# Optimization experiments

Hardware: AMD Instinct MI355X
Metric: run time of the kernel (lower is better)

Reference implementation:

```python
import jax, jax.numpy as jnp
import numpy as np

DIM = 768
NUM_HEADS = 12
HEAD_DIM = DIM // NUM_HEADS
ROPE_BASE = 10000.0


def _rope_angles(height, width, head_dim, base):
    # 2D RoPE: first half of head_dim rotates with the row (y) position,
    # second half with the column (x) position.
    half = head_dim // 2            # dims per spatial axis
    quarter = half // 2             # rotation pair count per axis
    inv_freq = 1.0 / (base ** (jnp.arange(0, half, 2, dtype=jnp.float32) / half))  # [quarter]
    ys = jnp.arange(height, dtype=jnp.float32)
    xs = jnp.arange(width, dtype=jnp.float32)
    ang_y = ys[:, None] * inv_freq  # [H, quarter]
    ang_x = xs[:, None] * inv_freq  # [W, quarter]
    ay = jnp.broadcast_to(ang_y[:, None, :], (height, width, quarter)).reshape(height * width, quarter)
    ax = jnp.broadcast_to(ang_x[None, :, :], (height, width, quarter)).reshape(height * width, quarter)
    return ay, ax


def _rotate(t, ang):
    # t: [B, nh, N, half]; ang: [N, quarter]. Interleaved pair rotation.
    c, s = jnp.cos(ang), jnp.sin(ang)
    t1, t2 = t[..., 0::2], t[..., 1::2]
    r1 = t1 * c - t2 * s
    r2 = t1 * s + t2 * c
    return jnp.stack([r1, r2], axis=-1).reshape(t.shape)


def apply_2d_rope(t, height, width, base):
    # t: [B, nh, N, head_dim]
    hd = t.shape[-1]
    half = hd // 2
    ay, ax = _rope_angles(height, width, hd, base)
    return jnp.concatenate([_rotate(t[..., :half], ay), _rotate(t[..., half:], ax)], axis=-1)


def setup_inputs() -> dict:
    key = jax.random.key(0)
    ks = jax.random.split(key, 5)
    B, N = 16, 32 * 32
    x = jax.random.normal(ks[0], (B, N, DIM), dtype=jnp.float32)
    qkv_w = jax.random.normal(ks[1], (3 * DIM, DIM), dtype=jnp.float32) * (1.0 / np.sqrt(DIM))
    qkv_b = jnp.zeros((3 * DIM,), dtype=jnp.float32)
    proj_w = jax.random.normal(ks[2], (DIM, DIM), dtype=jnp.float32) * (1.0 / np.sqrt(DIM))
    proj_b = jnp.zeros((DIM,), dtype=jnp.float32)
    return {"x": x, "qkv_w": qkv_w, "qkv_b": qkv_b, "proj_w": proj_w,
            "proj_b": proj_b, "height": 32, "width": 32}


def reference(x, qkv_w, qkv_b, proj_w, proj_b, height, width):
    B, N, C = x.shape
    scale = 1.0 / np.sqrt(HEAD_DIM)
    qkv = x @ qkv_w.T + qkv_b                      # [B, N, 3*C]
    qkv = qkv.reshape(B, N, 3, NUM_HEADS, HEAD_DIM).transpose(2, 0, 3, 1, 4)
    q, k, v = qkv[0], qkv[1], qkv[2]               # [B, nh, N, hd]
    q = apply_2d_rope(q, height, width, ROPE_BASE)
    k = apply_2d_rope(k, height, width, ROPE_BASE)
    attn = jnp.einsum('bhnd,bhmd->bhnm', q, k) * scale
    attn = jax.nn.softmax(attn, axis=-1)
    out = jnp.einsum('bhnm,bhmd->bhnd', attn, v)   # [B, nh, N, hd]
    out = out.transpose(0, 2, 1, 3).reshape(B, N, C)
    return out @ proj_w.T + proj_b
```

## Files before the change

kernel.cpp:

```cpp
#include <hip/hip_runtime.h>
#include <hip/hip_bf16.h>

typedef _Float16 f16;
typedef _Float16 half8 __attribute__((ext_vector_type(8)));
typedef _Float16 half4 __attribute__((ext_vector_type(4)));
typedef float f32x4 __attribute__((ext_vector_type(4)));
typedef unsigned short u16;
typedef unsigned int u32;

#define AS_GLOBAL __attribute__((address_space(1)))
#define AS_LDS    __attribute__((address_space(3)))

static __device__ __forceinline__ f32x4 mfma_k32(half8 a, half8 b, f32x4 c) {
  return __builtin_amdgcn_mfma_f32_16x16x32_f16(a, b, c, 0, 0, 0);
}

static __device__ __forceinline__ void glds16(const void* g, void* l) {
  __builtin_amdgcn_global_load_lds((const AS_GLOBAL u32*)(unsigned long long)g,
                                   (AS_LDS u32*)l, 16, 0, 0);
}

__global__ __launch_bounds__(256) void cvt_kernel(const float* __restrict__ src,
                                                  f16* __restrict__ dst, int n) {
  long i = ((long)blockIdx.x * 256 + threadIdx.x) * 8;
  if (i + 8 <= n) {
    const float4 a = *(const float4*)(src + i);
    const float4 b = *(const float4*)(src + i + 4);
    union { uint4 v; f16 h[8]; } o;
    o.h[0] = (f16)a.x; o.h[1] = (f16)a.y; o.h[2] = (f16)a.z; o.h[3] = (f16)a.w;
    o.h[4] = (f16)b.x; o.h[5] = (f16)b.y; o.h[6] = (f16)b.z; o.h[7] = (f16)b.w;
    *(uint4*)(dst + i) = o.v;
  }
}

static __device__ __forceinline__ void gemm128(const f16* __restrict__ A, const f16* __restrict__ B,
                                               const int K, const long m0, const long n0,
                                               f16* As, f16* Bs, f32x4 acc[4][4]) {
  const int tid = threadIdx.x;
  const int lane = tid & 63, w = tid >> 6;
  const int l15 = lane & 15, qd = lane >> 4;
  const int wr = w >> 1, wc = w & 1;
  const int rs   = lane >> 2;
  const int kofs = (lane & 3) * 8;
  const f16* gA0 = A + (m0 + 32 * w + rs) * (long)K + kofs;
  const f16* gA1 = gA0 + 16 * (long)K;
  const f16* gB0 = B + (n0 + 32 * w + rs) * (long)K + kofs;
  const f16* gB1 = gB0 + 16 * (long)K;
  f16* lA0 = As + (32 * w) * 32;  f16* lA1 = lA0 + 512;
  f16* lB0 = Bs + (32 * w) * 32;  f16* lB1 = lB0 + 512;
  const int nIter = K >> 5;
  for (int kt = 0; kt < nIter; ++kt) {
    const int ko = kt * 32;
    glds16(gA0 + ko, lA0);
    glds16(gA1 + ko, lA1);
    glds16(gB0 + ko, lB0);
    glds16(gB1 + ko, lB1);
    __syncthreads();
    half8 a[4], b[4];
#pragma unroll
    for (int i = 0; i < 4; ++i)
      a[i] = *(const half8*)(As + (64 * wr + 16 * i + l15) * 32 + qd * 8);
#pragma unroll
    for (int j = 0; j < 4; ++j)
      b[j] = *(const half8*)(Bs + (64 * wc + 16 * j + l15) * 32 + qd * 8);
#pragma unroll
    for (int i = 0; i < 4; ++i)
#pragma unroll
      for (int j = 0; j < 4; ++j)
        acc[i][j] = mfma_k32(a[i], b[j], acc[i][j]);
    __syncthreads();
  }
}

__global__ __launch_bounds__(256) void qkv_kernel(const f16* __restrict__ X, const f16* __restrict__ W,
                                                  const float* __restrict__ bias,
                                                  f16* __restrict__ Qf, f16* __restrict__ Kf,
                                                  f16* __restrict__ Vf) {
  __shared__ __align__(16) f16 As[4096];
  __shared__ __align__(16) f16 Bs[4096];
  f32x4 acc[4][4];
#pragma unroll
  for (int i = 0; i < 4; ++i)
#pragma unroll
    for (int j = 0; j < 4; ++j) acc[i][j] = (f32x4){0.f, 0.f, 0.f, 0.f};
  const long m0 = (long)blockIdx.x * 128;
  const long n0 = (long)blockIdx.y * 128;
  gemm128(X, W, 768, m0, n0, As, Bs, acc);

  const int tid = threadIdx.x, lane = tid & 63, w = tid >> 6;
  const int l15 = lane & 15, qd = lane >> 4;
  const int wr = w >> 1, wc = w & 1;
  const int bb = (int)(m0 >> 10);
  const int slot = (int)(n0 >> 6) + wc;
  const int which = slot / 12, h = slot % 12;
  f16* dst0 = (which == 0) ? Qf : (which == 1) ? Kf : Vf;
  f16* dstbh = dst0 + ((long)(bb * 12 + h)) * 1024 * 64;
  const bool doRope = (which != 2);
  const bool isQ = (which == 0);
  const bool odd = (l15 & 1);
#pragma unroll
  for (int j = 0; j < 4; ++j) {
    const int d = 16 * j + l15;
    const int p = d >> 1;
    const float fr = exp2f(-0.8304820237218405f * (float)(p & 15));
    const bool useY = (p < 16);
    const float bv = bias[n0 + 64 * wc + d];
#pragma unroll
    for (int i = 0; i < 4; ++i) {
      const int nbase = (int)(m0 & 1023) + 64 * wr + 16 * i + qd * 4;
#pragma unroll
      for (int r = 0; r < 4; ++r) {
        const int n = nbase + r;
        float v = acc[i][j][r] + bv;
        if (doRope) {
          const float pv = __shfl_xor(v, 1, 64);
          const float pos = useY ? (float)(n >> 5) : (float)(n & 31);
          float sn, cn;
          __sincosf(pos * fr, &sn, &cn);
          float res = odd ? (pv * sn + v * cn) : (v * cn - pv * sn);
          if (isQ) res *= 0.18033688011112042f;
          v = res;
        }
        dstbh[(long)n * 64 + d] = (f16)v;
      }
    }
  }
}

__global__ __launch_bounds__(256) void attn_kernel(const f16* __restrict__ Qf, const f16* __restrict__ Kf,
                                                   const f16* __restrict__ Vf, f16* __restrict__ Aout) {
  const int lin = (int)blockIdx.x + ((int)blockIdx.y << 3);
  const int xcd = lin & 7, idx = lin >> 3;
  const int bh = xcd * 24 + (idx >> 3);
  const int qt = idx & 7;
  const int b = bh / 12, h = bh % 12;
  const int tid = threadIdx.x;
  const int lane = tid & 63, w = tid >> 6;
  const int l15 = lane & 15, qd = lane >> 4;

  __shared__ __align__(16) f16 Ks[64][72];
  __shared__ __align__(16) f16 Vts[64][72];
  __shared__ float wsum[128];

  const f16* Qg = Qf + ((long)bh * 1024 + qt * 128) * 64;
  const f16* Kg = Kf + (long)bh * 1024 * 64;
  const f16* Vg = Vf + (long)bh * 1024 * 64;

  half8 qb[2][2];
#pragma unroll
  for (int g = 0; g < 2; ++g)
#pragma unroll
    for (int dc = 0; dc < 2; ++dc)
      qb[g][dc] = *(const half8*)(Qg + (w * 32 + g * 16 + l15) * 64 + dc * 32 + qd * 8);

  float lsum[2] = {0.f, 0.f};
  f32x4 O[2][4];
#pragma unroll
  for (int g = 0; g < 2; ++g)
#pragma unroll
    for (int nt = 0; nt < 4; ++nt) O[g][nt] = (f32x4){0.f, 0.f, 0.f, 0.f};

  const int srow = tid >> 2, sch = (tid & 3) * 16;
  const f16* kgb = Kg + (long)srow * 64 + sch;
  const int sk0 = (tid & 31) * 2, scd = tid >> 5;
  const f16* vgb = Vg + (long)sk0 * 64 + scd * 8;
  uint4 kr0, kr1, vr0, vr1;

  kr0 = *(const uint4*)(kgb);
  kr1 = *(const uint4*)(kgb + 8);
  vr0 = *(const uint4*)(vgb);
  vr1 = *(const uint4*)(vgb + 64);

  for (int kt = 0; kt < 16; ++kt) {
    *(uint4*)(&Ks[srow][sch])     = kr0;
    *(uint4*)(&Ks[srow][sch + 8]) = kr1;
    {
      union { uint4 u; f16 hh[8]; } ua, ub;
      ua.u = vr0; ub.u = vr1;
#pragma unroll
      for (int i2 = 0; i2 < 8; ++i2) {
        union { u32 u; f16 hh[2]; } t2;
        t2.hh[0] = ua.hh[i2]; t2.hh[1] = ub.hh[i2];
        *(u32*)(&Vts[scd * 8 + i2][sk0]) = t2.u;
      }
    }
    __syncthreads();

    if (kt < 15) {
      const f16* kp = kgb + (kt + 1) * 4096;
      kr0 = *(const uint4*)(kp);
      kr1 = *(const uint4*)(kp + 8);
      const f16* vp = vgb + (kt + 1) * 4096;
      vr0 = *(const uint4*)(vp);
      vr1 = *(const uint4*)(vp + 64);
    }

    f32x4 S[2][4];
#pragma unroll
    for (int kb = 0; kb < 4; ++kb) {
      const half8 ka0 = *(const half8*)(&Ks[kb * 16 + l15][qd * 8]);
      const half8 ka1 = *(const half8*)(&Ks[kb * 16 + l15][32 + qd * 8]);
#pragma unroll
      for (int g = 0; g < 2; ++g) {
        f32x4 z = (f32x4){0.f, 0.f, 0.f, 0.f};
        z = mfma_k32(ka0, qb[g][0], z);
        z = mfma_k32(ka1, qb[g][1], z);
        S[g][kb] = z;
      }
    }

    half8 pa8[2][2];
#pragma unroll
    for (int g = 0; g < 2; ++g)
#pragma unroll
      for (int c = 0; c < 2; ++c) {
        const f32x4 s0 = S[g][2 * c], s1 = S[g][2 * c + 1];
        const float p0 = __builtin_amdgcn_exp2f(s0[0]);
        const float p1 = __builtin_amdgcn_exp2f(s0[1]);
        const float p2 = __builtin_amdgcn_exp2f(s0[2]);
        const float p3 = __builtin_amdgcn_exp2f(s0[3]);
        const float p4 = __builtin_amdgcn_exp2f(s1[0]);
        const float p5 = __builtin_amdgcn_exp2f(s1[1]);
        const float p6 = __builtin_amdgcn_exp2f(s1[2]);
        const float p7 = __builtin_amdgcn_exp2f(s1[3]);
        lsum[g] += ((p0 + p1) + (p2 + p3)) + ((p4 + p5) + (p6 + p7));
        half8 pk;
        pk[0] = (f16)p0; pk[1] = (f16)p1; pk[2] = (f16)p2; pk[3] = (f16)p3;
        pk[4] = (f16)p4; pk[5] = (f16)p5; pk[6] = (f16)p6; pk[7] = (f16)p7;
        pa8[g][c] = pk;
      }

#pragma unroll
    for (int nt = 0; nt < 4; ++nt) {
      half8 vv[2];
#pragma unroll
      for (int c = 0; c < 2; ++c) {
        const half4 v0 = *(const half4*)(&Vts[nt * 16 + l15][c * 32 + qd * 4]);
        const half4 v1 = *(const half4*)(&Vts[nt * 16 + l15][c * 32 + 16 + qd * 4]);
        vv[c] = __builtin_shufflevector(v0, v1, 0, 1, 2, 3, 4, 5, 6, 7);
      }
#pragma unroll
      for (int g = 0; g < 2; ++g) {
        O[g][nt] = mfma_k32(pa8[g][0], vv[0], O[g][nt]);
        O[g][nt] = mfma_k32(pa8[g][1], vv[1], O[g][nt]);
      }
    }
    __syncthreads();
  }

#pragma unroll
  for (int g = 0; g < 2; ++g) {
    float s = lsum[g];
    s += __shfl_xor(s, 16, 64);
    s += __shfl_xor(s, 32, 64);
    if (lane < 16) wsum[w * 32 + g * 16 + lane] = s;
  }
  __syncthreads();
  float inv[2][4];
#pragma unroll
  for (int g = 0; g < 2; ++g)
#pragma unroll
    for (int r = 0; r < 4; ++r)
      inv[g][r] = 1.f / wsum[w * 32 + g * 16 + qd * 4 + r];
#pragma unroll
  for (int g = 0; g < 2; ++g)
#pragma unroll
    for (int r = 0; r < 4; ++r) {
      const int n = qt * 128 + w * 32 + g * 16 + qd * 4 + r;
      f16* dst = Aout + ((long)b * 1024 + n) * 768 + h * 64;
#pragma unroll
      for (int nt = 0; nt < 4; ++nt)
        dst[nt * 16 + l15] = (f16)(O[g][nt][r] * inv[g][r]);
    }
}

__global__ __launch_bounds__(256) void proj_kernel(const f16* __restrict__ A, const f16* __restrict__ W,
                                                   const float* __restrict__ bias, float* __restrict__ out) {
  __shared__ __align__(16) f16 As[4096];
  __shared__ __align__(16) f16 Bs[4096];
  f32x4 acc[4][4];
#pragma unroll
  for (int i = 0; i < 4; ++i)
#pragma unroll
    for (int j = 0; j < 4; ++j) acc[i][j] = (f32x4){0.f, 0.f, 0.f, 0.f};
  const long m0 = (long)blockIdx.x * 128;
  const long n0 = (long)blockIdx.y * 128;
  gemm128(A, W, 768, m0, n0, As, Bs, acc);

  const int tid = threadIdx.x, lane = tid & 63, w = tid >> 6;
  const int l15 = lane & 15, qd = lane >> 4;
  const int wr = w >> 1, wc = w & 1;
#pragma unroll
  for (int j = 0; j < 4; ++j) {
    const int col = (int)n0 + 64 * wc + 16 * j + l15;
    const float bv = bias[col];
#pragma unroll
    for (int i = 0; i < 4; ++i) {
      const long m = m0 + 64 * wr + 16 * i + qd * 4;
#pragma unroll
      for (int r = 0; r < 4; ++r)
        out[(m + r) * 768 + col] = acc[i][j][r] + bv;
    }
  }
}

extern "C" void kernel_launch(void* const* d_in, const int* in_sizes, int n_in,
                              void* d_out, int out_size, void* d_ws, size_t ws_size,
                              hipStream_t stream) {
  const float* x_f    = (const float*)d_in[0];
  const float* qkvw_f = (const float*)d_in[1];
  const float* qkvb_f = (const float*)d_in[2];
  const float* projw_f= (const float*)d_in[3];
  const float* projb_f= (const float*)d_in[4];

  char* ws = (char*)d_ws;
  f16* xh   = (f16*)(ws + 0);
  f16* wqh  = (f16*)(ws + 25165824);
  f16* wph  = (f16*)(ws + 28704768);
  f16* Qf   = (f16*)(ws + 29884416);
  f16* Kf   = (f16*)(ws + 55050240);
  f16* Vf   = (f16*)(ws + 80216064);
  f16* Aout = (f16*)(ws + 0);

  cvt_kernel<<<6144, 256, 0, stream>>>(x_f, xh, 12582912);
  cvt_kernel<<<864, 256, 0, stream>>>(qkvw_f, wqh, 1769472);
  cvt_kernel<<<288, 256, 0, stream>>>(projw_f, wph, 589824);
  qkv_kernel<<<dim3(128, 18), 256, 0, stream>>>(xh, wqh, qkvb_f, Qf, Kf, Vf);
  attn_kernel<<<dim3(8, 192), 256, 0, stream>>>(Qf, Kf, Vf, Aout);
  proj_kernel<<<dim3(128, 6), 256, 0, stream>>>(Aout, wph, projb_f, (float*)d_out);
}
```

Before: 301.0 us.

## Double-buffer GEMM tiles with swizzled LDS and enlarge QKV tile to 256x256

Both GEMMs now use a 64-wide K step with double-buffered LDS, so the next tile is prefetched through global_load_lds while the current one feeds the MFMAs. Column offsets are XOR-swizzled to reduce LDS bank conflicts, and MFMA issue priority is raised around the compute block. The QKV projection moves to 256x256 tiles with 512 threads and 8x4 accumulators per wave to raise data reuse. In exchange it uses far more LDS (128KB per QKV block) and more registers, and launches only 576 blocks.

```diff
diff --git a/kernel.cpp b/kernel.cpp
--- a/kernel.cpp
+++ b/kernel.cpp
@@ -33,63 +33,134 @@
   }
 }
 
-static __device__ __forceinline__ void gemm128(const f16* __restrict__ A, const f16* __restrict__ B,
+static __device__ __forceinline__ void gemm256(const f16* __restrict__ A, const f16* __restrict__ B,
                                                const int K, const long m0, const long n0,
-                                               f16* As, f16* Bs, f32x4 acc[4][4]) {
+                                               f16* As, f16* Bs, f32x4 acc[8][4]) {
+  const int tid = threadIdx.x;
+  const int lane = tid & 63, w = tid >> 6;
+  const int l15 = lane & 15, qd = lane >> 4;
+  const int wr = w >> 2, wc = w & 3;
+  const int srow = tid >> 3;
+  const int scol_sw = ((tid & 7) * 8) ^ (((lane >> 5) & 1) << 4);
+  const f16* gA = A + (m0 + srow) * (long)K + scol_sw;
+  const f16* gB = B + (n0 + srow) * (long)K + scol_sw;
+  f16* lA = As + w * 512;
+  f16* lB = Bs + w * 512;
+  const int sx = ((l15 >> 2) & 1) << 4;
+  const int nT = K >> 6;
+#pragma unroll
+  for (int r = 0; r < 4; ++r) {
+    glds16(gA + (long)r * 64 * K, lA + r * 4096);
+    glds16(gB + (long)r * 64 * K, lB + r * 4096);
+  }
+  __syncthreads();
+  for (int t = 0; t < nT; ++t) {
+    const int cb = (t & 1) * 16384, nb = ((t + 1) & 1) * 16384;
+    if (t + 1 < nT) {
+      const long ko = (long)(t + 1) * 64;
+#pragma unroll
+      for (int r = 0; r < 4; ++r) {
+        glds16(gA + (long)r * 64 * K + ko, lA + nb + r * 4096);
+        glds16(gB + (long)r * 64 * K + ko, lB + nb + r * 4096);
+      }
+    }
+    const f16* ab = As + cb + (wr * 128 + l15) * 64;
+    const f16* bb = Bs + cb + (wc * 64 + l15) * 64;
+#pragma unroll
+    for (int s = 0; s < 2; ++s) {
+      const int kc = s * 32 + ((qd * 8) ^ sx);
+      half8 b[4];
+#pragma unroll
+      for (int j = 0; j < 4; ++j) b[j] = *(const half8*)(bb + j * 1024 + kc);
+#pragma unroll
+      for (int mh = 0; mh < 2; ++mh) {
+        half8 a[4];
+#pragma unroll
+        for (int i = 0; i < 4; ++i) a[i] = *(const half8*)(ab + mh * 4096 + i * 1024 + kc);
+        __builtin_amdgcn_s_setprio(1);
+#pragma unroll
+        for (int i = 0; i < 4; ++i)
+#pragma unroll
+          for (int j = 0; j < 4; ++j)
+            acc[mh * 4 + i][j] = mfma_k32(a[i], b[j], acc[mh * 4 + i][j]);
+        __builtin_amdgcn_s_setprio(0);
+      }
+    }
+    __syncthreads();
+  }
+}
+
+static __device__ __forceinline__ void gemm128db(const f16* __restrict__ A, const f16* __restrict__ B,
+                                                 const int K, const long m0, const long n0,
+                                                 f16* As, f16* Bs, f32x4 acc[4][4]) {
   const int tid = threadIdx.x;
   const int lane = tid & 63, w = tid >> 6;
   const int l15 = lane & 15, qd = lane >> 4;
   const int wr = w >> 1, wc = w & 1;
-  const int rs   = lane >> 2;
-  const int kofs = (lane & 3) * 8;
-  const f16* gA0 = A + (m0 + 32 * w + rs) * (long)K + kofs;
-  const f16* gA1 = gA0 + 16 * (long)K;
-  const f16* gB0 = B + (n0 + 32 * w + rs) * (long)K + kofs;
-  const f16* gB1 = gB0 + 16 * (long)K;
-  f16* lA0 = As + (32 * w) * 32;  f16* lA1 = lA0 + 512;
-  f16* lB0 = Bs + (32 * w) * 32;  f16* lB1 = lB0 + 512;
-  const int nIter = K >> 5;
-  for (int kt = 0; kt < nIter; ++kt) {
-    const int ko = kt * 32;
-    glds16(gA0 + ko, lA0);
-    glds16(gA1 + ko, lA1);
-    glds16(gB0 + ko, lB0);
-    glds16(gB1 + ko, lB1);
+  const int srow = tid >> 3;
+  const int scol_sw = ((tid & 7) * 8) ^ (((lane >> 5) & 1) << 4);
+  const f16* gA = A + (m0 + srow) * (long)K + scol_sw;
+  const f16* gB = B + (n0 + srow) * (long)K + scol_sw;
+  f16* lA = As + w * 512;
+  f16* lB = Bs + w * 512;
+  const int sx = ((l15 >> 2) & 1) << 4;
+  const int nT = K >> 6;
+#pragma unroll
+  for (int r = 0; r < 4; ++r) {
+    glds16(gA + (long)r * 32 * K, lA + r * 2048);
+    glds16(gB + (long)r * 32 * K, lB + r * 2048);
+  }
+  __syncthreads();
+  for (int t = 0; t < nT; ++t) {
+    const int cb = (t & 1) * 8192, nb = ((t + 1) & 1) * 8192;
+    if (t + 1 < nT) {
+      const long ko = (long)(t + 1) * 64;
+#pragma unroll
+      for (int r = 0; r < 4; ++r) {
+        glds16(gA + (long)r * 32 * K + ko, lA + nb + r * 2048);
+        glds16(gB + (long)r * 32 * K + ko, lB + nb + r * 2048);
+      }
+    }
+    const f16* ab = As + cb + (wr * 64 + l15) * 64;
+    const f16* bb = Bs + cb + (wc * 64 + l15) * 64;
+#pragma unroll
+    for (int s = 0; s < 2; ++s) {
+      const int kc = s * 32 + ((qd * 8) ^ sx);
+      half8 a[4], b[4];
+#pragma unroll
+      for (int j = 0; j < 4; ++j) b[j] = *(const half8*)(bb + j * 1024 + kc);
+#pragma unroll
+      for (int i = 0; i < 4; ++i) a[i] = *(const half8*)(ab + i * 1024 + kc);
+      __builtin_amdgcn_s_setprio(1);
+#pragma unroll
+      for (int i = 0; i < 4; ++i)
+#pragma unroll
+        for (int j = 0; j < 4; ++j)
+          acc[i][j] = mfma_k32(a[i], b[j], acc[i][j]);
+      __builtin_amdgcn_s_setprio(0);
+    }
     __syncthreads();
-    half8 a[4], b[4];
-#pragma unroll
-    for (int i = 0; i < 4; ++i)
-      a[i] = *(const half8*)(As + (64 * wr + 16 * i + l15) * 32 + qd * 8);
-#pragma unroll
-    for (int j = 0; j < 4; ++j)
-      b[j] = *(const half8*)(Bs + (64 * wc + 16 * j + l15) * 32 + qd * 8);
-#pragma unroll
-    for (int i = 0; i < 4; ++i)
-#pragma unroll
-      for (int j = 0; j < 4; ++j)
-        acc[i][j] = mfma_k32(a[i], b[j], acc[i][j]);
-    __syncthreads();
-  }
-}
-
-__global__ __launch_bounds__(256) void qkv_kernel(const f16* __restrict__ X, const f16* __restrict__ W,
-                                                  const float* __restrict__ bias,
-                                                  f16* __restrict__ Qf, f16* __restrict__ Kf,
-                                                  f16* __restrict__ Vf) {
-  __shared__ __align__(16) f16 As[4096];
-  __shared__ __align__(16) f16 Bs[4096];
-  f32x4 acc[4][4];
-#pragma unroll
-  for (int i = 0; i < 4; ++i)
+  }
+}
+
+__global__ __launch_bounds__(512, 2) void qkv_kernel(const f16* __restrict__ X, const f16* __restrict__ W,
+                                                     const float* __restrict__ bias,
+                                                     f16* __restrict__ Qf, f16* __restrict__ Kf,
+                                                     f16* __restrict__ Vf) {
+  __shared__ __align__(16) f16 As[32768];
+  __shared__ __align__(16) f16 Bs[32768];
+  f32x4 acc[8][4];
+#pragma unroll
+  for (int i = 0; i < 8; ++i)
 #pragma unroll
     for (int j = 0; j < 4; ++j) acc[i][j] = (f32x4){0.f, 0.f, 0.f, 0.f};
-  const long m0 = (long)blockIdx.x * 128;
-  const long n0 = (long)blockIdx.y * 128;
-  gemm128(X, W, 768, m0, n0, As, Bs, acc);
+  const long m0 = (long)blockIdx.x * 256;
+  const long n0 = (long)blockIdx.y * 256;
+  gemm256(X, W, 768, m0, n0, As, Bs, acc);
 
   const int tid = threadIdx.x, lane = tid & 63, w = tid >> 6;
   const int l15 = lane & 15, qd = lane >> 4;
-  const int wr = w >> 1, wc = w & 1;
+  const int wr = w >> 2, wc = w & 3;
   const int bb = (int)(m0 >> 10);
   const int slot = (int)(n0 >> 6) + wc;
   const int which = slot / 12, h = slot % 12;
@@ -106,8 +177,8 @@
     const bool useY = (p < 16);
     const float bv = bias[n0 + 64 * wc + d];
 #pragma unroll
-    for (int i = 0; i < 4; ++i) {
-      const int nbase = (int)(m0 & 1023) + 64 * wr + 16 * i + qd * 4;
+    for (int i = 0; i < 8; ++i) {
+      const int nbase = (int)(m0 & 1023) + 128 * wr + 16 * i + qd * 4;
 #pragma unroll
       for (int r = 0; r < 4; ++r) {
         const int n = nbase + r;
@@ -276,8 +347,8 @@
 
 __global__ __launch_bounds__(256) void proj_kernel(const f16* __restrict__ A, const f16* __restrict__ W,
                                                    const float* __restrict__ bias, float* __restrict__ out) {
-  __shared__ __align__(16) f16 As[4096];
-  __shared__ __align__(16) f16 Bs[4096];
+  __shared__ __align__(16) f16 As[16384];
+  __shared__ __align__(16) f16 Bs[16384];
   f32x4 acc[4][4];
 #pragma unroll
   for (int i = 0; i < 4; ++i)
@@ -285,7 +356,7 @@
     for (int j = 0; j < 4; ++j) acc[i][j] = (f32x4){0.f, 0.f, 0.f, 0.f};
   const long m0 = (long)blockIdx.x * 128;
   const long n0 = (long)blockIdx.y * 128;
-  gemm128(A, W, 768, m0, n0, As, Bs, acc);
+  gemm128db(A, W, 768, m0, n0, As, Bs, acc);
 
   const int tid = threadIdx.x, lane = tid & 63, w = tid >> 6;
   const int l15 = lane & 15, qd = lane >> 4;
@@ -325,7 +396,7 @@
   cvt_kernel<<<6144, 256, 0, stream>>>(x_f, xh, 12582912);
   cvt_kernel<<<864, 256, 0, stream>>>(qkvw_f, wqh, 1769472);
   cvt_kernel<<<288, 256, 0, stream>>>(projw_f, wph, 589824);
-  qkv_kernel<<<dim3(128, 18), 256, 0, stream>>>(xh, wqh, qkvb_f, Qf, Kf, Vf);
+  qkv_kernel<<<dim3(64, 9), 512, 0, stream>>>(xh, wqh, qkvb_f, Qf, Kf, Vf);
   attn_kernel<<<dim3(8, 192), 256, 0, stream>>>(Qf, Kf, Vf, Aout);
   proj_kernel<<<dim3(128, 6), 256, 0, stream>>>(Aout, wph, projb_f, (float*)d_out);
 }
```

Result: slower. 317.7 us (+5.6%).

## Triple-buffer GEMM tiles with async LDS loads and XOR swizzle

Applied to the files above, without the earlier changes.

Replaces the single-buffered GEMM main loop used by the QKV and projection kernels with a three-stage pipeline. Global-to-LDS loads run two tiles ahead, gated by vmcnt waits and one barrier per iteration instead of two. The LDS layout is XOR-swizzled to cut bank conflicts, and MFMA issue is interleaved with fragment reads under raised wave priority. LDS use per block triples, which may lower occupancy.

```diff
diff --git a/kernel.cpp b/kernel.cpp
--- a/kernel.cpp
+++ b/kernel.cpp
@@ -33,51 +33,89 @@
   }
 }
 
-static __device__ __forceinline__ void gemm128(const f16* __restrict__ A, const f16* __restrict__ B,
-                                               const int K, const long m0, const long n0,
-                                               f16* As, f16* Bs, f32x4 acc[4][4]) {
+static __device__ __forceinline__ void gemm128p(const f16* __restrict__ A, const f16* __restrict__ B,
+                                                const int K, const long m0, const long n0,
+                                                f16* As, f16* Bs, f32x4 acc[4][4]) {
   const int tid = threadIdx.x;
   const int lane = tid & 63, w = tid >> 6;
   const int l15 = lane & 15, qd = lane >> 4;
   const int wr = w >> 1, wc = w & 1;
-  const int rs   = lane >> 2;
-  const int kofs = (lane & 3) * 8;
-  const f16* gA0 = A + (m0 + 32 * w + rs) * (long)K + kofs;
-  const f16* gA1 = gA0 + 16 * (long)K;
-  const f16* gB0 = B + (n0 + 32 * w + rs) * (long)K + kofs;
-  const f16* gB1 = gB0 + 16 * (long)K;
-  f16* lA0 = As + (32 * w) * 32;  f16* lA1 = lA0 + 512;
-  f16* lB0 = Bs + (32 * w) * 32;  f16* lB1 = lB0 + 512;
-  const int nIter = K >> 5;
-  for (int kt = 0; kt < nIter; ++kt) {
-    const int ko = kt * 32;
-    glds16(gA0 + ko, lA0);
-    glds16(gA1 + ko, lA1);
-    glds16(gB0 + ko, lB0);
-    glds16(gB1 + ko, lB1);
-    __syncthreads();
-    half8 a[4], b[4];
-#pragma unroll
-    for (int i = 0; i < 4; ++i)
-      a[i] = *(const half8*)(As + (64 * wr + 16 * i + l15) * 32 + qd * 8);
-#pragma unroll
-    for (int j = 0; j < 4; ++j)
-      b[j] = *(const half8*)(Bs + (64 * wc + 16 * j + l15) * 32 + qd * 8);
-#pragma unroll
-    for (int i = 0; i < 4; ++i)
-#pragma unroll
-      for (int j = 0; j < 4; ++j)
-        acc[i][j] = mfma_k32(a[i], b[j], acc[i][j]);
-    __syncthreads();
-  }
+  const int srow = w * 16 + (lane >> 2);
+  const int sg   = ((lane & 3) ^ ((lane >> 3) & 3)) * 8;
+  const f16* gA0 = A + (m0 + srow) * (long)K + sg;
+  const f16* gA1 = gA0 + 64 * (long)K;
+  const f16* gB0 = B + (n0 + srow) * (long)K + sg;
+  const f16* gB1 = gB0 + 64 * (long)K;
+  f16* lA = As + w * 512;
+  f16* lB = Bs + w * 512;
+  const int rg   = (qd ^ ((l15 >> 1) & 3)) * 8;
+  const int arow = (wr * 64 + l15) * 32;
+  const int brow = (wc * 64 + l15) * 32;
+  const int nT = K >> 5;
+
+#define STAGE(t) { const long ko = (long)(t) * 32;                         \
+    f16* dA = lA + ((t) % 3) * 4096; f16* dB = lB + ((t) % 3) * 4096;      \
+    glds16(gA0 + ko, dA); glds16(gA1 + ko, dA + 2048);                     \
+    glds16(gB0 + ko, dB); glds16(gB1 + ko, dB + 2048); }
+
+  STAGE(0); STAGE(1);
+  asm volatile("s_waitcnt vmcnt(4)" ::: "memory");
+  __builtin_amdgcn_sched_barrier(0);
+  __builtin_amdgcn_s_barrier();
+  __builtin_amdgcn_sched_barrier(0);
+#pragma unroll
+  for (int t = 0; t < nT; ++t) {
+    if (t + 2 < nT) STAGE(t + 2);
+    const f16* cA = As + (t % 3) * 4096;
+    const f16* cB = Bs + (t % 3) * 4096;
+    half8 a0[2], a1[2], b0[2], b1[2];
+    a0[0] = *(const half8*)(cA + arow + rg);
+    a0[1] = *(const half8*)(cA + arow + 512 + rg);
+    b0[0] = *(const half8*)(cB + brow + rg);
+    b0[1] = *(const half8*)(cB + brow + 512 + rg);
+    __builtin_amdgcn_s_setprio(1);
+    acc[0][0] = mfma_k32(a0[0], b0[0], acc[0][0]);
+    acc[0][1] = mfma_k32(a0[0], b0[1], acc[0][1]);
+    acc[1][0] = mfma_k32(a0[1], b0[0], acc[1][0]);
+    acc[1][1] = mfma_k32(a0[1], b0[1], acc[1][1]);
+    __builtin_amdgcn_s_setprio(0);
+    b1[0] = *(const half8*)(cB + brow + 1024 + rg);
+    b1[1] = *(const half8*)(cB + brow + 1536 + rg);
+    __builtin_amdgcn_s_setprio(1);
+    acc[0][2] = mfma_k32(a0[0], b1[0], acc[0][2]);
+    acc[0][3] = mfma_k32(a0[0], b1[1], acc[0][3]);
+    acc[1][2] = mfma_k32(a0[1], b1[0], acc[1][2]);
+    acc[1][3] = mfma_k32(a0[1], b1[1], acc[1][3]);
+    __builtin_amdgcn_s_setprio(0);
+    a1[0] = *(const half8*)(cA + arow + 1024 + rg);
+    a1[1] = *(const half8*)(cA + arow + 1536 + rg);
+    __builtin_amdgcn_s_setprio(1);
+    acc[2][2] = mfma_k32(a1[0], b1[0], acc[2][2]);
+    acc[2][3] = mfma_k32(a1[0], b1[1], acc[2][3]);
+    acc[3][2] = mfma_k32(a1[1], b1[0], acc[3][2]);
+    acc[3][3] = mfma_k32(a1[1], b1[1], acc[3][3]);
+    acc[2][0] = mfma_k32(a1[0], b0[0], acc[2][0]);
+    acc[2][1] = mfma_k32(a1[0], b0[1], acc[2][1]);
+    acc[3][0] = mfma_k32(a1[1], b0[0], acc[3][0]);
+    acc[3][1] = mfma_k32(a1[1], b0[1], acc[3][1]);
+    __builtin_amdgcn_s_setprio(0);
+    if (t < nT - 1) {
+      if (t == nT - 2) { asm volatile("s_waitcnt vmcnt(0)" ::: "memory"); }
+      else             { asm volatile("s_waitcnt vmcnt(4)" ::: "memory"); }
+      __builtin_amdgcn_sched_barrier(0);
+      __builtin_amdgcn_s_barrier();
+      __builtin_amdgcn_sched_barrier(0);
+    }
+  }
+#undef STAGE
 }
 
 __global__ __launch_bounds__(256) void qkv_kernel(const f16* __restrict__ X, const f16* __restrict__ W,
                                                   const float* __restrict__ bias,
                                                   f16* __restrict__ Qf, f16* __restrict__ Kf,
                                                   f16* __restrict__ Vf) {
-  __shared__ __align__(16) f16 As[4096];
-  __shared__ __align__(16) f16 Bs[4096];
+  __shared__ __align__(16) f16 As[12288];
+  __shared__ __align__(16) f16 Bs[12288];
   f32x4 acc[4][4];
 #pragma unroll
   for (int i = 0; i < 4; ++i)
@@ -85,7 +123,7 @@
     for (int j = 0; j < 4; ++j) acc[i][j] = (f32x4){0.f, 0.f, 0.f, 0.f};
   const long m0 = (long)blockIdx.x * 128;
   const long n0 = (long)blockIdx.y * 128;
-  gemm128(X, W, 768, m0, n0, As, Bs, acc);
+  gemm128p(X, W, 768, m0, n0, As, Bs, acc);
 
   const int tid = threadIdx.x, lane = tid & 63, w = tid >> 6;
   const int l15 = lane & 15, qd = lane >> 4;
@@ -276,8 +314,8 @@
 
 __global__ __launch_bounds__(256) void proj_kernel(const f16* __restrict__ A, const f16* __restrict__ W,
                                                    const float* __restrict__ bias, float* __restrict__ out) {
-  __shared__ __align__(16) f16 As[4096];
-  __shared__ __align__(16) f16 Bs[4096];
+  __shared__ __align__(16) f16 As[12288];
+  __shared__ __align__(16) f16 Bs[12288];
   f32x4 acc[4][4];
 #pragma unroll
   for (int i = 0; i < 4; ++i)
@@ -285,7 +323,7 @@
     for (int j = 0; j < 4; ++j) acc[i][j] = (f32x4){0.f, 0.f, 0.f, 0.f};
   const long m0 = (long)blockIdx.x * 128;
   const long n0 = (long)blockIdx.y * 128;
-  gemm128(A, W, 768, m0, n0, As, Bs, acc);
+  gemm128p(A, W, 768, m0, n0, As, Bs, acc);
 
   const int tid = threadIdx.x, lane = tid & 63, w = tid >> 6;
   const int l15 = lane & 15, qd = lane >> 4;
```

Result: no change. 303.4 us (+0.8%).
